# Kernel tuning notes

Hardware: AMD Instinct MI355X
Metric: run time of the kernel (lower is better)

## Reference

```python
import jax, jax.numpy as jnp
import numpy as np

FILL = -1024.0


def setup_inputs() -> dict:
    key = jax.random.key(0)
    ks = jax.random.split(key, 8)
    B, Q, K, D, KD, VD = 4, 4096, 4096, 512, 64, 64
    s = 0.02  # small init scale for numeric sanity
    return {
        "x": jax.random.normal(ks[0], (B, Q, D), dtype=jnp.float32),
        "buffer": jax.random.normal(ks[1], (B, K, D), dtype=jnp.float32),
        "mask": jax.random.randint(ks[2], (B, Q, K), 0, 2) > 0,
        "Wq": jax.random.normal(ks[3], (KD, D), dtype=jnp.float32) * s,
        "bq": jnp.zeros((KD,), dtype=jnp.float32),
        "Wk": jax.random.normal(ks[4], (KD, D), dtype=jnp.float32) * s,
        "bk": jnp.zeros((KD,), dtype=jnp.float32),
        "Wv": jax.random.normal(ks[5], (VD, D), dtype=jnp.float32) * s,
        "bv": jnp.zeros((VD,), dtype=jnp.float32),
    }


def reference(x, buffer, mask, Wq, bq, Wk, bk, Wv, bv):
    key_dim = Wq.shape[0]
    query = x @ Wq.T + bq          # [B, Q, KD]
    keys = buffer @ Wk.T + bk      # [B, K, KD]
    vals = buffer @ Wv.T + bv      # [B, K, VD]
    logits = jnp.einsum('bqd,bkd->bqk', query, keys) / np.sqrt(key_dim).astype(np.float32)
    logits = jnp.where(mask, logits, FILL)
    # stable softmax (same math as exp(x - max) / sum)
    probs = jax.nn.softmax(logits, axis=-1)
    read = jnp.einsum('bqk,bkd->bqd', probs, vals)  # [B, Q, VD]
    return read
```

## Files before the change

### kernel.cpp

```cpp
#include <hip/hip_runtime.h>
#include <hip/hip_bf16.h>

typedef float f32x4 __attribute__((ext_vector_type(4)));
typedef __bf16 bf16x8 __attribute__((ext_vector_type(8)));
typedef unsigned long long u64;
typedef u64 u64x2 __attribute__((ext_vector_type(2)));

#define NB 4
#define NQ 4096
#define NK 4096
#define DIM 512
#define KD 64
#define PKW 128
#define NG64 (1 << 20)
#define PACK_BLOCKS 2048
#define PACK_WAVES (PACK_BLOCKS * 4)

__global__ __launch_bounds__(256, 8) void pack_kernel(
        const int* __restrict__ mask, unsigned* __restrict__ pk) {
    const int tid = threadIdx.x;
    const int w = tid >> 6, l = tid & 63;
    const int wid = blockIdx.x * 4 + w;
    u64* pk64 = (u64*)pk;
#pragma unroll 1
    for (int g0 = wid * 8; g0 < NG64; g0 += PACK_WAVES * 8) {
        const int* mb = mask + (long)g0 * 64 + l;
        int m[8];
#pragma unroll
        for (int j = 0; j < 8; j++) m[j] = mb[j * 64];
        u64 bb[8];
#pragma unroll
        for (int j = 0; j < 8; j++) bb[j] = __ballot(m[j] != 0);
        if (l == 0) {
#pragma unroll
            for (int j = 0; j < 4; j++) {
                u64x2 v = {bb[2 * j], bb[2 * j + 1]};
                *(u64x2*)(pk64 + g0 + 2 * j) = v;
            }
        }
    }
}

__device__ inline bf16x8 load_cvt8(const float* __restrict__ p) {
    float4 f0 = *(const float4*)p;
    float4 f1 = *(const float4*)(p + 4);
    bf16x8 r;
    r[0] = (__bf16)f0.x; r[1] = (__bf16)f0.y; r[2] = (__bf16)f0.z; r[3] = (__bf16)f0.w;
    r[4] = (__bf16)f1.x; r[5] = (__bf16)f1.y; r[6] = (__bf16)f1.z; r[7] = (__bf16)f1.w;
    return r;
}

__global__ __launch_bounds__(256, 4) void proj_kernel(
        const float* __restrict__ x, const float* __restrict__ buf,
        const float* __restrict__ Wq, const float* __restrict__ bq,
        const float* __restrict__ Wk, const float* __restrict__ bk,
        const float* __restrict__ Wv, const float* __restrict__ bv,
        __bf16* __restrict__ Qb, __bf16* __restrict__ Kb, __bf16* __restrict__ Vt) {
    __shared__ __align__(16) float ps[4][32][66];

    const int tid = threadIdx.x;
    const int w = tid >> 6, l = tid & 63;
    const int lr = l & 15, lk = l >> 4;
    const int rg = w >> 1, kh = w & 1;
    const bool is_q = blockIdx.x < 512;
    const int blk = is_q ? blockIdx.x : blockIdx.x - 512;
    const long rowbase = (long)blk * 32 + rg * 16;
    const int kbase = kh * 256;

    if (is_q) {
        f32x4 acc[4] = {};
#pragma unroll 4
        for (int kk = 0; kk < 256; kk += 32) {
            bf16x8 a = load_cvt8(x + (rowbase + lr) * DIM + kbase + kk + lk * 8);
#pragma unroll
            for (int nb = 0; nb < 4; nb++) {
                bf16x8 bw = load_cvt8(Wq + (long)(nb * 16 + lr) * DIM + kbase + kk + lk * 8);
                acc[nb] = __builtin_amdgcn_mfma_f32_16x16x32_bf16(a, bw, acc[nb], 0, 0, 0);
            }
        }
#pragma unroll
        for (int nb = 0; nb < 4; nb++)
#pragma unroll
            for (int i = 0; i < 4; i++)
                ps[kh * 2][rg * 16 + lk * 4 + i][nb * 16 + lr] = acc[nb][i];
        __syncthreads();
        for (int e = tid; e < 2048; e += 256) {
            int row = e >> 6, col = e & 63;
            float v = (ps[0][row][col] + ps[2][row][col] + bq[col]) * 0.125f;
            Qb[((long)blk * 32 + row) * KD + col] = (__bf16)v;
        }
    } else {
        f32x4 acck[4] = {}, accv[4] = {};
#pragma unroll 2
        for (int kk = 0; kk < 256; kk += 32) {
            bf16x8 a = load_cvt8(buf + (rowbase + lr) * DIM + kbase + kk + lk * 8);
#pragma unroll
            for (int nb = 0; nb < 4; nb++) {
                bf16x8 bwk = load_cvt8(Wk + (long)(nb * 16 + lr) * DIM + kbase + kk + lk * 8);
                bf16x8 bwv = load_cvt8(Wv + (long)(nb * 16 + lr) * DIM + kbase + kk + lk * 8);
                acck[nb] = __builtin_amdgcn_mfma_f32_16x16x32_bf16(a, bwk, acck[nb], 0, 0, 0);
                accv[nb] = __builtin_amdgcn_mfma_f32_16x16x32_bf16(a, bwv, accv[nb], 0, 0, 0);
            }
        }
#pragma unroll
        for (int nb = 0; nb < 4; nb++)
#pragma unroll
            for (int i = 0; i < 4; i++) {
                ps[kh * 2 + 0][rg * 16 + lk * 4 + i][nb * 16 + lr] = acck[nb][i];
                ps[kh * 2 + 1][rg * 16 + lk * 4 + i][nb * 16 + lr] = accv[nb][i];
            }
        __syncthreads();
        for (int e = tid; e < 2048; e += 256) {
            int row = e >> 6, col = e & 63;
            float v = ps[0][row][col] + ps[2][row][col] + bk[col];
            Kb[((long)blk * 32 + row) * KD + col] = (__bf16)v;
        }
        for (int e = tid; e < 2048; e += 256) {
            int row = e & 31, col = e >> 5;
            float v = ps[1][row][col] + ps[3][row][col] + bv[col];
            long grow = (long)blk * 32 + row;
            int b = (int)(grow >> 12), kidx = (int)(grow & 4095);
            Vt[((long)b * KD + col) * NK + kidx] = (__bf16)v;
        }
    }
}

__global__ __launch_bounds__(512, 4) void attn_kernel(
        const __bf16* __restrict__ Qb, const __bf16* __restrict__ Kb,
        const __bf16* __restrict__ Vt, const unsigned* __restrict__ pk,
        float* __restrict__ out) {
    __shared__ __align__(16) char smem[36864];

    const int tid = threadIdx.x;
    const int w = tid >> 6, l = tid & 63;
    const int lr = l & 15, lk = l >> 4;
    const int orig = blockIdx.x;
    const int xcd = orig & 7, slot = orig >> 3;
    const int b = xcd >> 1;
    const int q0 = ((xcd & 1) * 128 + slot) * 16;
    const int k0 = w * 512;

    const __bf16* Qp = Qb + ((long)b * NQ + q0) * KD;
    const __bf16* Kp = Kb + (long)b * NK * KD;
    const __bf16* Vp = Vt + (long)b * KD * NK;
    const unsigned* mp = pk + ((long)b * NQ + q0) * PKW;

    __bf16 (*pl0)[72] = (__bf16(*)[72])(smem + w * 4608);
    __bf16 (*pl1)[72] = (__bf16(*)[72])(smem + w * 4608 + 2304);

    bf16x8 qa[2];
#pragma unroll
    for (int ks = 0; ks < 2; ks++)
        qa[ks] = *(const bf16x8*)(Qp + (long)lr * KD + ks * 32 + lk * 8);

    f32x4 o[4] = {};
    float l_i[4] = {0.f, 0.f, 0.f, 0.f};

    auto tile = [&](int kt, __bf16 (*pl)[72]) {
        f32x4 s[4] = {};
#pragma unroll
        for (int ks = 0; ks < 2; ks++)
#pragma unroll
            for (int nb = 0; nb < 4; nb++) {
                bf16x8 kb = *(const bf16x8*)(Kp + (long)(kt + nb * 16 + lr) * KD + ks * 32 + lk * 8);
                s[nb] = __builtin_amdgcn_mfma_f32_16x16x32_bf16(qa[ks], kb, s[nb], 0, 0, 0);
            }
        unsigned mw0[4], mw1[4];
#pragma unroll
        for (int i = 0; i < 4; i++) {
            uint2 mwv = *(const uint2*)(mp + (long)(lk * 4 + i) * PKW + (kt >> 5));
            mw0[i] = mwv.x; mw1[i] = mwv.y;
        }
#pragma unroll
        for (int nb = 0; nb < 4; nb++) {
            const unsigned bit = (unsigned)((nb * 16 + lr) & 31);
#pragma unroll
            for (int i = 0; i < 4; i++) {
                unsigned wv = (nb < 2) ? mw0[i] : mw1[i];
                float e = __expf(s[nb][i]);
                float p = ((wv >> bit) & 1u) ? e : 0.0f;
                __bf16 pb = (__bf16)p;
                pl[lk * 4 + i][nb * 16 + lr] = pb;
                l_i[i] += (float)pb;
            }
        }
#pragma unroll
        for (int ks = 0; ks < 2; ks++) {
            bf16x8 pa = *(const bf16x8*)&pl[lr][ks * 32 + lk * 8];
#pragma unroll
            for (int nb = 0; nb < 4; nb++) {
                bf16x8 vb = *(const bf16x8*)(Vp + (long)(nb * 16 + lr) * NK + kt + ks * 32 + lk * 8);
                o[nb] = __builtin_amdgcn_mfma_f32_16x16x32_bf16(pa, vb, o[nb], 0, 0, 0);
            }
        }
    };

#pragma unroll 1
    for (int kt = k0; kt < k0 + 512; kt += 128) {
        tile(kt, pl0);
        tile(kt + 64, pl1);
    }

#pragma unroll
    for (int i = 0; i < 4; i++) {
        float v = l_i[i];
        v += __shfl_xor(v, 1);
        v += __shfl_xor(v, 2);
        v += __shfl_xor(v, 4);
        v += __shfl_xor(v, 8);
        l_i[i] = v;
    }

    __syncthreads();
    float* o_s = (float*)smem;
    float* ml  = (float*)(smem + 8 * 16 * 66 * 4);
#pragma unroll
    for (int nb = 0; nb < 4; nb++)
#pragma unroll
        for (int i = 0; i < 4; i++)
            o_s[(w * 16 + lk * 4 + i) * 66 + nb * 16 + lr] = o[nb][i];
    if (lr == 0) {
#pragma unroll
        for (int i = 0; i < 4; i++)
            ml[w * 16 + lk * 4 + i] = l_i[i];
    }
    __syncthreads();
    for (int e = tid; e < 1024; e += 512) {
        int row = e >> 6, col = e & 63;
        float L = 0.f, O = 0.f;
#pragma unroll
        for (int ww = 0; ww < 8; ww++) {
            L += ml[ww * 16 + row];
            O += o_s[(ww * 16 + row) * 66 + col];
        }
        out[((long)b * NQ + q0 + row) * KD + col] = O / L;
    }
}

extern "C" void kernel_launch(void* const* d_in, const int* in_sizes, int n_in,
                              void* d_out, int out_size, void* d_ws, size_t ws_size,
                              hipStream_t stream) {
    const float* x      = (const float*)d_in[0];
    const float* buffer = (const float*)d_in[1];
    const int*   mask   = (const int*)d_in[2];
    const float* Wq     = (const float*)d_in[3];
    const float* bq     = (const float*)d_in[4];
    const float* Wk     = (const float*)d_in[5];
    const float* bk     = (const float*)d_in[6];
    const float* Wv     = (const float*)d_in[7];
    const float* bv     = (const float*)d_in[8];
    float* out = (float*)d_out;

    unsigned* pk = (unsigned*)d_ws;
    __bf16* Qb = (__bf16*)((char*)d_ws + (size_t)NB * NQ * PKW * 4);
    __bf16* Kb = Qb + (size_t)NB * NQ * KD;
    __bf16* Vt = Kb + (size_t)NB * NK * KD;

    pack_kernel<<<dim3(PACK_BLOCKS), dim3(256), 0, stream>>>(mask, pk);
    proj_kernel<<<dim3(1024), dim3(256), 0, stream>>>(x, buffer, Wq, bq, Wk, bk, Wv, bv, Qb, Kb, Vt);
    attn_kernel<<<dim3(NB * (NQ / 16)), dim3(512), 0, stream>>>(Qb, Kb, Vt, pk, out);
}
```

Before: 264.1 us.

## Split attention block into two query groups with four key quarters each

The attention kernel now gives each 512-thread block 32 query rows: two 16-row query groups, each split across four waves that cover 1024 keys apiece. The old layout was 16 rows with eight waves of 512 keys. This halves the grid, lengthens each wave's key loop, and drops the XCD-aware block-to-batch mapping. It also halves the cross-wave reduction fan-in. The mask-word loads are moved ahead of the QK MFMAs to start them earlier, and the K/V projection loop unroll goes from 2 to 4. Tradeoffs: fewer blocks, less intra-block key parallelism per query row, and possibly worse L2 locality without the XCD mapping.

```diff
diff --git a/kernel.cpp b/kernel.cpp
--- a/kernel.cpp
+++ b/kernel.cpp
@@ -91,7 +91,7 @@
         }
     } else {
         f32x4 acck[4] = {}, accv[4] = {};
-#pragma unroll 2
+#pragma unroll 4
         for (int kk = 0; kk < 256; kk += 32) {
             bf16x8 a = load_cvt8(buf + (rowbase + lr) * DIM + kbase + kk + lk * 8);
 #pragma unroll
@@ -134,16 +134,17 @@
     const int tid = threadIdx.x;
     const int w = tid >> 6, l = tid & 63;
     const int lr = l & 15, lk = l >> 4;
-    const int orig = blockIdx.x;
-    const int xcd = orig & 7, slot = orig >> 3;
-    const int b = xcd >> 1;
-    const int q0 = ((xcd & 1) * 128 + slot) * 16;
-    const int k0 = w * 512;
-
-    const __bf16* Qp = Qb + ((long)b * NQ + q0) * KD;
+    const int b = blockIdx.x >> 7;
+    const int q0 = (blockIdx.x & 127) * 32;
+    const int qg = w & 1;
+    const int kq = w >> 1;
+    const int qw = q0 + qg * 16;
+    const int k0 = kq * 1024;
+
+    const __bf16* Qp = Qb + ((long)b * NQ + qw) * KD;
     const __bf16* Kp = Kb + (long)b * NK * KD;
     const __bf16* Vp = Vt + (long)b * KD * NK;
-    const unsigned* mp = pk + ((long)b * NQ + q0) * PKW;
+    const unsigned* mp = pk + ((long)b * NQ + qw) * PKW;
 
     __bf16 (*pl0)[72] = (__bf16(*)[72])(smem + w * 4608);
     __bf16 (*pl1)[72] = (__bf16(*)[72])(smem + w * 4608 + 2304);
@@ -157,20 +158,20 @@
     float l_i[4] = {0.f, 0.f, 0.f, 0.f};
 
     auto tile = [&](int kt, __bf16 (*pl)[72]) {
-        f32x4 s[4] = {};
-#pragma unroll
-        for (int ks = 0; ks < 2; ks++)
-#pragma unroll
-            for (int nb = 0; nb < 4; nb++) {
-                bf16x8 kb = *(const bf16x8*)(Kp + (long)(kt + nb * 16 + lr) * KD + ks * 32 + lk * 8);
-                s[nb] = __builtin_amdgcn_mfma_f32_16x16x32_bf16(qa[ks], kb, s[nb], 0, 0, 0);
-            }
         unsigned mw0[4], mw1[4];
 #pragma unroll
         for (int i = 0; i < 4; i++) {
             uint2 mwv = *(const uint2*)(mp + (long)(lk * 4 + i) * PKW + (kt >> 5));
             mw0[i] = mwv.x; mw1[i] = mwv.y;
         }
+        f32x4 s[4] = {};
+#pragma unroll
+        for (int ks = 0; ks < 2; ks++)
+#pragma unroll
+            for (int nb = 0; nb < 4; nb++) {
+                bf16x8 kb = *(const bf16x8*)(Kp + (long)(kt + nb * 16 + lr) * KD + ks * 32 + lk * 8);
+                s[nb] = __builtin_amdgcn_mfma_f32_16x16x32_bf16(qa[ks], kb, s[nb], 0, 0, 0);
+            }
 #pragma unroll
         for (int nb = 0; nb < 4; nb++) {
             const unsigned bit = (unsigned)((nb * 16 + lr) & 31);
@@ -196,7 +197,7 @@
     };
 
 #pragma unroll 1
-    for (int kt = k0; kt < k0 + 512; kt += 128) {
+    for (int kt = k0; kt < k0 + 1024; kt += 128) {
         tile(kt, pl0);
         tile(kt + 64, pl1);
     }
@@ -214,26 +215,29 @@
     __syncthreads();
     float* o_s = (float*)smem;
     float* ml  = (float*)(smem + 8 * 16 * 66 * 4);
+    const int part = qg * 4 + kq;
 #pragma unroll
     for (int nb = 0; nb < 4; nb++)
 #pragma unroll
         for (int i = 0; i < 4; i++)
-            o_s[(w * 16 + lk * 4 + i) * 66 + nb * 16 + lr] = o[nb][i];
+            o_s[(part * 16 + lk * 4 + i) * 66 + nb * 16 + lr] = o[nb][i];
     if (lr == 0) {
 #pragma unroll
         for (int i = 0; i < 4; i++)
-            ml[w * 16 + lk * 4 + i] = l_i[i];
+            ml[part * 16 + lk * 4 + i] = l_i[i];
     }
     __syncthreads();
-    for (int e = tid; e < 1024; e += 512) {
-        int row = e >> 6, col = e & 63;
+    for (int e = tid; e < 2048; e += 512) {
+        int row32 = e >> 6, col = e & 63;
+        int g = row32 >> 4, row = row32 & 15;
         float L = 0.f, O = 0.f;
 #pragma unroll
-        for (int ww = 0; ww < 8; ww++) {
-            L += ml[ww * 16 + row];
-            O += o_s[(ww * 16 + row) * 66 + col];
-        }
-        out[((long)b * NQ + q0 + row) * KD + col] = O / L;
+        for (int kk = 0; kk < 4; kk++) {
+            int p = g * 4 + kk;
+            L += ml[p * 16 + row];
+            O += o_s[(p * 16 + row) * 66 + col];
+        }
+        out[((long)b * NQ + q0 + row32) * KD + col] = O / L;
     }
 }
 
@@ -258,5 +262,5 @@
 
     pack_kernel<<<dim3(PACK_BLOCKS), dim3(256), 0, stream>>>(mask, pk);
     proj_kernel<<<dim3(1024), dim3(256), 0, stream>>>(x, buffer, Wq, bq, Wk, bk, Wv, bv, Qb, Kb, Vt);
-    attn_kernel<<<dim3(NB * (NQ / 16)), dim3(512), 0, stream>>>(Qb, Kb, Vt, pk, out);
-}
+    attn_kernel<<<dim3(NB * (NQ / 32)), dim3(512), 0, stream>>>(Qb, Kb, Vt, pk, out);
+}
```

New measurement: 264.7 us. No clear change (+0.2%).
